# Optimization experiments

Measured on AMD Instinct MI355X. Metric: run time of the kernel, lower is better.

The kernel has to match this reference:

```python
import jax, jax.numpy as jnp
import numpy as np

N_LETTERS = 256
EMBED_DIM = 1024
HIDDEN_DIM = 2048
SEQ_LEN = 4096


def setup_inputs() -> dict:
    key = jax.random.key(0)
    ks = jax.random.split(key, 8)
    s_e = 1.0 / np.sqrt(EMBED_DIM)
    s_h = 1.0 / np.sqrt(HIDDEN_DIM)
    return {
        "input_ids": jax.random.randint(ks[0], (SEQ_LEN,), 0, N_LETTERS, dtype=jnp.int64)
        if jax.config.jax_enable_x64 else jax.random.randint(ks[0], (SEQ_LEN,), 0, N_LETTERS, dtype=jnp.int32),
        "h0": jnp.zeros((1, 1, HIDDEN_DIM), jnp.float32),
        "c0": jnp.zeros((1, 1, HIDDEN_DIM), jnp.float32),
        "W_emb": jax.random.normal(ks[1], (N_LETTERS, EMBED_DIM), jnp.float32),
        "W_ih": jax.random.normal(ks[2], (4 * HIDDEN_DIM, EMBED_DIM), jnp.float32) * s_e,
        "W_hh": jax.random.normal(ks[3], (4 * HIDDEN_DIM, HIDDEN_DIM), jnp.float32) * s_h,
        "b_ih": jnp.zeros((4 * HIDDEN_DIM,), jnp.float32),
        "b_hh": jnp.zeros((4 * HIDDEN_DIM,), jnp.float32),
        "W_out": jax.random.normal(ks[4], (N_LETTERS, HIDDEN_DIM), jnp.float32) * s_h,
        "b_out": jnp.zeros((N_LETTERS,), jnp.float32),
    }


def reference(input_ids, h0, c0, W_emb, W_ih, W_hh, b_ih, b_hh, W_out, b_out):
    H = W_hh.shape[1]
    emb = W_emb[input_ids]                       # [L, E]
    # Precompute the input-side gate projections for all timesteps (batched GEMM).
    x_gates = emb @ W_ih.T + (b_ih + b_hh)       # [L, 4H]

    def step(carry, xg):
        h, c = carry                             # [H], [H]
        gates = xg + W_hh @ h                    # [4H], PyTorch order i,f,g,o
        i = jax.nn.sigmoid(gates[0 * H:1 * H])
        f = jax.nn.sigmoid(gates[1 * H:2 * H])
        g = jnp.tanh(gates[2 * H:3 * H])
        o = jax.nn.sigmoid(gates[3 * H:4 * H])
        c_new = f * c + i * g
        h_new = o * jnp.tanh(c_new)
        return (h_new, c_new), h_new

    (hL, cL), hs = jax.lax.scan(step, (h0[0, 0], c0[0, 0]), x_gates)  # hs: [L, H]
    logits = hs @ W_out.T + b_out                # [L, n_letters]
    # Dropout(p=0.1) is identity in eval mode.
    out = jax.nn.log_softmax(jax.nn.relu(logits), axis=-1)
    return out, hL[None, None, :], cL[None, None, :]
```

## Files before the change

kernel.cpp:

```cpp
#include <hip/hip_runtime.h>
#include <hip/hip_bf16.h>

#define SEQ 4096
#define EMB 1024
#define HID 2048
#define G4  8192
#define NL  256

typedef __attribute__((ext_vector_type(8))) short bf16x8;
typedef __attribute__((ext_vector_type(4))) float f32x4;

static __device__ __forceinline__ unsigned short f2bf(float f) {
    unsigned int x = __builtin_bit_cast(unsigned int, f);
    return (unsigned short)((x + 0x7FFFu + ((x >> 16) & 1u)) >> 16);
}
static __device__ __forceinline__ float bf2f(unsigned short u) {
    return __builtin_bit_cast(float, ((unsigned int)u) << 16);
}

__global__ __launch_bounds__(256) void k_f2b(const float* __restrict__ in,
                                             unsigned short* __restrict__ out, int n) {
    int i = (blockIdx.x * 256 + threadIdx.x) * 4;
    if (i < n) {
        float4 v = *(const float4*)&in[i];
        ushort4 u;
        u.x = f2bf(v.x); u.y = f2bf(v.y); u.z = f2bf(v.z); u.w = f2bf(v.w);
        *(ushort4*)&out[i] = u;
    }
}

__global__ __launch_bounds__(256) void k_emb(const int* __restrict__ ids,
                                             const float* __restrict__ W_emb,
                                             unsigned short* __restrict__ out) {
    int t = blockIdx.x;
    int e0 = threadIdx.x * 4;
    const float4 v = *(const float4*)&W_emb[(size_t)ids[t] * EMB + e0];
    ushort4 u;
    u.x = f2bf(v.x); u.y = f2bf(v.y); u.z = f2bf(v.z); u.w = f2bf(v.w);
    *(ushort4*)&out[(size_t)t * EMB + e0] = u;
}

#define BM 128
#define BN 128
#define BK 32
__global__ __launch_bounds__(256) void k_gemm_bt(
    const unsigned short* __restrict__ A, const unsigned short* __restrict__ B,
    const float* __restrict__ bias1, const float* __restrict__ bias2,
    float* __restrict__ Cf, unsigned short* __restrict__ Cb,
    int M, int N, int K)
{
    __shared__ unsigned short As[BM * BK];
    __shared__ unsigned short Bs[BN * BK];
    const int bm = blockIdx.x * BM;
    const int bn = blockIdx.y * BN;
    const int tid = threadIdx.x;
    const int wave = tid >> 6, lane = tid & 63;
    const int wm = (wave & 1) * 64, wn = (wave >> 1) * 64;
    const int row16 = lane & 15, quad = lane >> 4;

    f32x4 acc[4][4];
#pragma unroll
    for (int i = 0; i < 4; ++i)
#pragma unroll
        for (int j = 0; j < 4; ++j) acc[i][j] = (f32x4){0.f, 0.f, 0.f, 0.f};

    for (int k0 = 0; k0 < K; k0 += BK) {
        __syncthreads();
#pragma unroll
        for (int s = 0; s < 2; ++s) {
            int c = tid + s * 256;
            int r = c >> 2, col = (c & 3) * 8;
            *(uint4*)&As[r * BK + col] = *(const uint4*)&A[(size_t)(bm + r) * K + k0 + col];
            *(uint4*)&Bs[r * BK + col] = *(const uint4*)&B[(size_t)(bn + r) * K + k0 + col];
        }
        __syncthreads();
        bf16x8 af[4], bfr[4];
#pragma unroll
        for (int i = 0; i < 4; ++i) {
            af[i]  = *(const bf16x8*)&As[(wm + i * 16 + row16) * BK + quad * 8];
            bfr[i] = *(const bf16x8*)&Bs[(wn + i * 16 + row16) * BK + quad * 8];
        }
#pragma unroll
        for (int i = 0; i < 4; ++i)
#pragma unroll
            for (int j = 0; j < 4; ++j)
                acc[i][j] = __builtin_amdgcn_mfma_f32_16x16x32_bf16(af[i], bfr[j], acc[i][j], 0, 0, 0);
    }

#pragma unroll
    for (int j = 0; j < 4; ++j) {
        int col = bn + wn + j * 16 + row16;
        float bsum = (bias1 ? bias1[col] : 0.f) + (bias2 ? bias2[col] : 0.f);
#pragma unroll
        for (int i = 0; i < 4; ++i) {
#pragma unroll
            for (int r = 0; r < 4; ++r) {
                int row = bm + wm + i * 16 + quad * 4 + r;
                float v = acc[i][j][r] + bsum;
                if (Cf) Cf[(size_t)row * N + col] = v;
                else    Cb[(size_t)row * N + col] = f2bf(v);
            }
        }
    }
}

#define LSTM_LDS 90112
__global__ __launch_bounds__(1024, 1) void k_lstm(
    const unsigned short* __restrict__ Whhb,
    const unsigned short* __restrict__ xg,
    const float* __restrict__ h0, const float* __restrict__ c0,
    unsigned short* __restrict__ hsb,
    float* __restrict__ outHC,
    unsigned long long* __restrict__ hcomm)
{
    extern __shared__ char smem[];
    unsigned short* hl = (unsigned short*)smem;
    unsigned int*  hl32 = (unsigned int*)smem;
    float* LDSp = (float*)(smem + 4096);
    float* gsum = (float*)(smem + 4096 + 1024);

    const int b = blockIdx.x, tid = threadIdx.x;
    const int wave = tid >> 6, lane = tid & 63;
    const int sub = lane & 15, quad = lane >> 4;
    const int rg = wave & 1, kset = wave >> 1;

    const int q = rg * 2 + (sub >> 3);
    const int j = sub & 7;
    const unsigned short* wsrc =
        Whhb + ((size_t)(q * HID + b * 8 + j)) * HID + kset * 8 * 32 + quad * 8;
    bf16x8 afr[8];
#pragma unroll
    for (int i = 0; i < 8; ++i)
        afr[i] = *(const bf16x8*)(wsrc + i * 32);

    float creg = 0.f;
    if (tid < 8) creg = c0[b * 8 + tid];

    for (int t = 0; t < SEQ; ++t) {
        float xq0 = 0.f, xq1 = 0.f, xq2 = 0.f, xq3 = 0.f;
        if (tid < 8) {
            const unsigned short* xr = xg + (size_t)t * G4 + b * 8 + tid;
            xq0 = bf2f(xr[0]);
            xq1 = bf2f(xr[2048]);
            xq2 = bf2f(xr[4096]);
            xq3 = bf2f(xr[6144]);
        }

        if (t == 0) {
            if (tid < 512) {
                float4 v = *(const float4*)&h0[tid * 4];
                ushort4 u;
                u.x = f2bf(v.x); u.y = f2bf(v.y); u.z = f2bf(v.z); u.w = f2bf(v.w);
                *(ushort4*)&hl[tid * 4] = u;
            }
        } else {
            const unsigned long long* src = hcomm + (size_t)((t - 1) & 1) * 1024;
            const unsigned tag = (unsigned)t;
            unsigned long long x;
            for (;;) {
                x = __hip_atomic_load(&src[tid], __ATOMIC_RELAXED, __HIP_MEMORY_SCOPE_AGENT);
                if ((unsigned)(x >> 32) == tag) break;
                __builtin_amdgcn_s_sleep(1);
            }
            hl32[tid] = (unsigned int)x;
        }
        __syncthreads();

        f32x4 acc0 = (f32x4){0.f, 0.f, 0.f, 0.f};
        f32x4 acc1 = (f32x4){0.f, 0.f, 0.f, 0.f};
#pragma unroll
        for (int i = 0; i < 8; i += 2) {
            bf16x8 h0f = *(const bf16x8*)&hl[(kset * 8 + i) * 32 + quad * 8];
            bf16x8 h1f = *(const bf16x8*)&hl[(kset * 8 + i + 1) * 32 + quad * 8];
            acc0 = __builtin_amdgcn_mfma_f32_16x16x32_bf16(afr[i],     h0f, acc0, 0, 0, 0);
            acc1 = __builtin_amdgcn_mfma_f32_16x16x32_bf16(afr[i + 1], h1f, acc1, 0, 0, 0);
        }
        f32x4 acc = acc0 + acc1;
        if (sub == 0) {
#pragma unroll
            for (int r = 0; r < 4; ++r)
                LDSp[(rg * 16 + quad * 4 + r) * 8 + kset] = acc[r];
        }
        __syncthreads();

        if (tid < 256) {
            float v = LDSp[tid];
            v += __shfl_xor(v, 1); v += __shfl_xor(v, 2); v += __shfl_xor(v, 4);
            if ((tid & 7) == 0) gsum[tid >> 3] = v;
        }
        __syncthreads();

        if (tid < 8) {
            float gi = gsum[tid]      + xq0;
            float gf = gsum[8 + tid]  + xq1;
            float gg = gsum[16 + tid] + xq2;
            float go = gsum[24 + tid] + xq3;
            float i_ = 1.f / (1.f + __expf(-gi));
            float f_ = 1.f / (1.f + __expf(-gf));
            float g_ = tanhf(gg);
            float o_ = 1.f / (1.f + __expf(-go));
            float cn = f_ * creg + i_ * g_;
            float hn = o_ * tanhf(cn);
            creg = cn;
            unsigned hv = (unsigned)f2bf(hn);
            unsigned ov = (unsigned)__shfl_xor((int)hv, 1);
            if ((tid & 1) == 0) {
                unsigned data = hv | (ov << 16);
                __hip_atomic_store(&hcomm[(size_t)(t & 1) * 1024 + b * 4 + (tid >> 1)],
                                   (((unsigned long long)(unsigned)(t + 1)) << 32) | data,
                                   __ATOMIC_RELAXED, __HIP_MEMORY_SCOPE_AGENT);
            }
            hsb[(size_t)t * HID + b * 8 + tid] = f2bf(hn);
            if (t == SEQ - 1) {
                outHC[b * 8 + tid] = hn;
                outHC[HID + b * 8 + tid] = cn;
            }
        }
    }
}

__global__ __launch_bounds__(256) void k_softmax(const float* __restrict__ logits,
                                                 float* __restrict__ out) {
    int row = blockIdx.x * 4 + (threadIdx.x >> 6);
    int lane = threadIdx.x & 63;
    const float* Lr = logits + (size_t)row * NL;
    float4 v = *(const float4*)&Lr[lane * 4];
    v.x = fmaxf(v.x, 0.f); v.y = fmaxf(v.y, 0.f);
    v.z = fmaxf(v.z, 0.f); v.w = fmaxf(v.w, 0.f);
    float m = fmaxf(fmaxf(v.x, v.y), fmaxf(v.z, v.w));
#pragma unroll
    for (int off = 32; off > 0; off >>= 1) m = fmaxf(m, __shfl_xor(m, off));
    float e = __expf(v.x - m) + __expf(v.y - m) + __expf(v.z - m) + __expf(v.w - m);
#pragma unroll
    for (int off = 32; off > 0; off >>= 1) e += __shfl_xor(e, off);
    float ls = __logf(e) + m;
    float4 o;
    o.x = v.x - ls; o.y = v.y - ls; o.z = v.z - ls; o.w = v.w - ls;
    *(float4*)&out[(size_t)row * NL + lane * 4] = o;
}

extern "C" void kernel_launch(void* const* d_in, const int* in_sizes, int n_in,
                              void* d_out, int out_size, void* d_ws, size_t ws_size,
                              hipStream_t stream) {
    const int*   ids   = (const int*)d_in[0];
    const float* h0    = (const float*)d_in[1];
    const float* c0    = (const float*)d_in[2];
    const float* W_emb = (const float*)d_in[3];
    const float* W_ih  = (const float*)d_in[4];
    const float* W_hh  = (const float*)d_in[5];
    const float* b_ih  = (const float*)d_in[6];
    const float* b_hh  = (const float*)d_in[7];
    const float* W_out = (const float*)d_in[8];
    const float* b_out = (const float*)d_in[9];
    float* out = (float*)d_out;

    char* ws = (char*)d_ws;
    unsigned short* xg    = (unsigned short*)(ws);
    unsigned short* hsb   = (unsigned short*)(ws + 67108864);
    unsigned short* Wihb  = (unsigned short*)(ws + 83886080);
    unsigned short* embb  = (unsigned short*)(ws + 100663296);
    unsigned short* Woutb = (unsigned short*)(ws + 109051904);
    float*          logit = (float*)(ws + 110100480);
    unsigned short* Whhb  = (unsigned short*)(ws + 114294784);
    unsigned long long* hcomm = (unsigned long long*)(ws + 147849216);

    k_f2b<<<(G4 * EMB / 4 + 255) / 256, 256, 0, stream>>>(W_ih, Wihb, G4 * EMB);
    k_f2b<<<(NL * HID / 4 + 255) / 256, 256, 0, stream>>>(W_out, Woutb, NL * HID);
    k_f2b<<<(G4 * HID / 4 + 255) / 256, 256, 0, stream>>>(W_hh, Whhb, G4 * HID);
    k_emb<<<SEQ, 256, 0, stream>>>(ids, W_emb, embb);

    dim3 g1(SEQ / BM, G4 / BN);
    k_gemm_bt<<<g1, 256, 0, stream>>>(embb, Wihb, b_ih, b_hh, nullptr, xg, SEQ, G4, EMB);

    hipFuncSetAttribute((const void*)k_lstm, hipFuncAttributeMaxDynamicSharedMemorySize, LSTM_LDS);
    k_lstm<<<256, 1024, LSTM_LDS, stream>>>(Whhb, xg, h0, c0, hsb, out + (size_t)SEQ * NL, hcomm);

    dim3 g2(SEQ / BM, NL / BN);
    k_gemm_bt<<<g2, 256, 0, stream>>>(hsb, Woutb, b_out, nullptr, logit, nullptr, SEQ, NL, HID);

    k_softmax<<<SEQ / 4, 256, 0, stream>>>(logit, out);
}
```

Measured before the change: 11.40 ms.

## Load recurrent h directly into MFMA fragments and cut LSTM step barriers

Each wave now covers a 128-wide K slice for both row groups and polls the tagged hcomm words straight into registers as MFMA B fragments. This removes the LDS staging of h and the barrier that followed it. The cross-wave reduction is merged into a single wave reading padded LDS rows, which drops one __syncthreads per timestep. Gate activations switch to exp-based fast sigmoid and tanh. In exchange, every wave spins on 16 global atomic loads with no sleep, and tanh loses a little accuracy.

```diff
diff --git a/kernel.cpp b/kernel.cpp
--- a/kernel.cpp
+++ b/kernel.cpp
@@ -16,6 +16,15 @@
 }
 static __device__ __forceinline__ float bf2f(unsigned short u) {
     return __builtin_bit_cast(float, ((unsigned int)u) << 16);
+}
+static __device__ __forceinline__ unsigned long long aload(const unsigned long long* p) {
+    return __hip_atomic_load(p, __ATOMIC_RELAXED, __HIP_MEMORY_SCOPE_AGENT);
+}
+static __device__ __forceinline__ float fsigm(float x) {
+    return 1.f / (1.f + __expf(-x));
+}
+static __device__ __forceinline__ float ftanh(float x) {
+    return 1.f - 2.f / (__expf(2.f * x) + 1.f);
 }
 
 __global__ __launch_bounds__(256) void k_f2b(const float* __restrict__ in,
@@ -114,106 +123,131 @@
     unsigned long long* __restrict__ hcomm)
 {
     extern __shared__ char smem[];
-    unsigned short* hl = (unsigned short*)smem;
-    unsigned int*  hl32 = (unsigned int*)smem;
-    float* LDSp = (float*)(smem + 4096);
-    float* gsum = (float*)(smem + 4096 + 1024);
+    float* LDSp = (float*)smem;
 
     const int b = blockIdx.x, tid = threadIdx.x;
     const int wave = tid >> 6, lane = tid & 63;
     const int sub = lane & 15, quad = lane >> 4;
-    const int rg = wave & 1, kset = wave >> 1;
-
-    const int q = rg * 2 + (sub >> 3);
-    const int j = sub & 7;
-    const unsigned short* wsrc =
-        Whhb + ((size_t)(q * HID + b * 8 + j)) * HID + kset * 8 * 32 + quad * 8;
-    bf16x8 afr[8];
-#pragma unroll
-    for (int i = 0; i < 8; ++i)
-        afr[i] = *(const bf16x8*)(wsrc + i * 32);
+
+    const int qa = (sub >> 3), qb = 2 + (sub >> 3), j = sub & 7;
+    const unsigned short* wa = Whhb + ((size_t)(qa * HID + b * 8 + j)) * HID + wave * 128 + quad * 8;
+    const unsigned short* wb = Whhb + ((size_t)(qb * HID + b * 8 + j)) * HID + wave * 128 + quad * 8;
+    bf16x8 afrA[4], afrB[4];
+#pragma unroll
+    for (int c = 0; c < 4; ++c) {
+        afrA[c] = *(const bf16x8*)(wa + c * 32);
+        afrB[c] = *(const bf16x8*)(wb + c * 32);
+    }
 
     float creg = 0.f;
     if (tid < 8) creg = c0[b * 8 + tid];
 
     for (int t = 0; t < SEQ; ++t) {
         float xq0 = 0.f, xq1 = 0.f, xq2 = 0.f, xq3 = 0.f;
-        if (tid < 8) {
-            const unsigned short* xr = xg + (size_t)t * G4 + b * 8 + tid;
+        if (wave == 0 && lane < 8) {
+            const unsigned short* xr = xg + (size_t)t * G4 + b * 8 + lane;
             xq0 = bf2f(xr[0]);
             xq1 = bf2f(xr[2048]);
             xq2 = bf2f(xr[4096]);
             xq3 = bf2f(xr[6144]);
         }
 
-        if (t == 0) {
-            if (tid < 512) {
-                float4 v = *(const float4*)&h0[tid * 4];
-                ushort4 u;
-                u.x = f2bf(v.x); u.y = f2bf(v.y); u.z = f2bf(v.z); u.w = f2bf(v.w);
-                *(ushort4*)&hl[tid * 4] = u;
-            }
-        } else {
-            const unsigned long long* src = hcomm + (size_t)((t - 1) & 1) * 1024;
-            const unsigned tag = (unsigned)t;
-            unsigned long long x;
-            for (;;) {
-                x = __hip_atomic_load(&src[tid], __ATOMIC_RELAXED, __HIP_MEMORY_SCOPE_AGENT);
-                if ((unsigned)(x >> 32) == tag) break;
-                __builtin_amdgcn_s_sleep(1);
-            }
-            hl32[tid] = (unsigned int)x;
-        }
-        __syncthreads();
-
         f32x4 acc0 = (f32x4){0.f, 0.f, 0.f, 0.f};
         f32x4 acc1 = (f32x4){0.f, 0.f, 0.f, 0.f};
-#pragma unroll
-        for (int i = 0; i < 8; i += 2) {
-            bf16x8 h0f = *(const bf16x8*)&hl[(kset * 8 + i) * 32 + quad * 8];
-            bf16x8 h1f = *(const bf16x8*)&hl[(kset * 8 + i + 1) * 32 + quad * 8];
-            acc0 = __builtin_amdgcn_mfma_f32_16x16x32_bf16(afr[i],     h0f, acc0, 0, 0, 0);
-            acc1 = __builtin_amdgcn_mfma_f32_16x16x32_bf16(afr[i + 1], h1f, acc1, 0, 0, 0);
-        }
-        f32x4 acc = acc0 + acc1;
+
+        if (t == 0) {
+#pragma unroll
+            for (int c = 0; c < 4; ++c) {
+                const float* hp = h0 + wave * 128 + c * 32 + quad * 8;
+                float4 va = *(const float4*)hp;
+                float4 vb = *(const float4*)(hp + 4);
+                uint4 d;
+                d.x = (unsigned)f2bf(va.x) | ((unsigned)f2bf(va.y) << 16);
+                d.y = (unsigned)f2bf(va.z) | ((unsigned)f2bf(va.w) << 16);
+                d.z = (unsigned)f2bf(vb.x) | ((unsigned)f2bf(vb.y) << 16);
+                d.w = (unsigned)f2bf(vb.z) | ((unsigned)f2bf(vb.w) << 16);
+                bf16x8 hf = __builtin_bit_cast(bf16x8, d);
+                acc0 = __builtin_amdgcn_mfma_f32_16x16x32_bf16(afrA[c], hf, acc0, 0, 0, 0);
+                acc1 = __builtin_amdgcn_mfma_f32_16x16x32_bf16(afrB[c], hf, acc1, 0, 0, 0);
+            }
+        } else {
+            const unsigned long long* base =
+                hcomm + (size_t)((t - 1) & 1) * 1024 + wave * 64 + quad * 4;
+            const unsigned tag = (unsigned)t;
+            unsigned long long w[16];
+            for (;;) {
+#pragma unroll
+                for (int c = 0; c < 4; ++c)
+#pragma unroll
+                    for (int i = 0; i < 4; ++i)
+                        w[c * 4 + i] = aload(base + c * 16 + i);
+                bool ok = true;
+#pragma unroll
+                for (int k = 0; k < 16; ++k) ok &= ((unsigned)(w[k] >> 32) == tag);
+                if (ok) break;
+            }
+#pragma unroll
+            for (int c = 0; c < 4; ++c) {
+                uint4 d;
+                d.x = (unsigned)w[c * 4 + 0];
+                d.y = (unsigned)w[c * 4 + 1];
+                d.z = (unsigned)w[c * 4 + 2];
+                d.w = (unsigned)w[c * 4 + 3];
+                bf16x8 hf = __builtin_bit_cast(bf16x8, d);
+                acc0 = __builtin_amdgcn_mfma_f32_16x16x32_bf16(afrA[c], hf, acc0, 0, 0, 0);
+                acc1 = __builtin_amdgcn_mfma_f32_16x16x32_bf16(afrB[c], hf, acc1, 0, 0, 0);
+            }
+        }
+
+        __syncthreads();
         if (sub == 0) {
 #pragma unroll
-            for (int r = 0; r < 4; ++r)
-                LDSp[(rg * 16 + quad * 4 + r) * 8 + kset] = acc[r];
+            for (int r = 0; r < 4; ++r) {
+                LDSp[(quad * 4 + r) * 20 + wave]        = acc0[r];
+                LDSp[(16 + quad * 4 + r) * 20 + wave]   = acc1[r];
+            }
         }
         __syncthreads();
 
-        if (tid < 256) {
-            float v = LDSp[tid];
-            v += __shfl_xor(v, 1); v += __shfl_xor(v, 2); v += __shfl_xor(v, 4);
-            if ((tid & 7) == 0) gsum[tid >> 3] = v;
-        }
-        __syncthreads();
-
-        if (tid < 8) {
-            float gi = gsum[tid]      + xq0;
-            float gf = gsum[8 + tid]  + xq1;
-            float gg = gsum[16 + tid] + xq2;
-            float go = gsum[24 + tid] + xq3;
-            float i_ = 1.f / (1.f + __expf(-gi));
-            float f_ = 1.f / (1.f + __expf(-gf));
-            float g_ = tanhf(gg);
-            float o_ = 1.f / (1.f + __expf(-go));
-            float cn = f_ * creg + i_ * g_;
-            float hn = o_ * tanhf(cn);
-            creg = cn;
-            unsigned hv = (unsigned)f2bf(hn);
-            unsigned ov = (unsigned)__shfl_xor((int)hv, 1);
-            if ((tid & 1) == 0) {
-                unsigned data = hv | (ov << 16);
-                __hip_atomic_store(&hcomm[(size_t)(t & 1) * 1024 + b * 4 + (tid >> 1)],
-                                   (((unsigned long long)(unsigned)(t + 1)) << 32) | data,
-                                   __ATOMIC_RELAXED, __HIP_MEMORY_SCOPE_AGENT);
-            }
-            hsb[(size_t)t * HID + b * 8 + tid] = f2bf(hn);
-            if (t == SEQ - 1) {
-                outHC[b * 8 + tid] = hn;
-                outHC[HID + b * 8 + tid] = cn;
+        if (wave == 0) {
+            float g = 0.f;
+            if (lane < 32) {
+                const float* rp = LDSp + lane * 20;
+                f32x4 s = *(const f32x4*)rp;
+                s += *(const f32x4*)(rp + 4);
+                s += *(const f32x4*)(rp + 8);
+                s += *(const f32x4*)(rp + 12);
+                g = s[0] + s[1] + s[2] + s[3];
+            }
+            float gF = __shfl(g, 8 + lane);
+            float gG = __shfl(g, 16 + lane);
+            float gO = __shfl(g, 24 + lane);
+            if (lane < 8) {
+                float gi = g  + xq0;
+                float gf = gF + xq1;
+                float gg = gG + xq2;
+                float go = gO + xq3;
+                float i_ = fsigm(gi);
+                float f_ = fsigm(gf);
+                float g_ = ftanh(gg);
+                float o_ = fsigm(go);
+                float cn = f_ * creg + i_ * g_;
+                float hn = o_ * ftanh(cn);
+                creg = cn;
+                unsigned hv = (unsigned)f2bf(hn);
+                unsigned pv = (unsigned)__shfl((int)hv, lane ^ 1);
+                if (!(lane & 1)) {
+                    unsigned long long wrd =
+                        (((unsigned long long)(unsigned)(t + 1)) << 32)
+                        | (unsigned long long)((pv << 16) | hv);
+                    __hip_atomic_store(&hcomm[(size_t)(t & 1) * 1024 + b * 4 + (lane >> 1)],
+                                       wrd, __ATOMIC_RELAXED, __HIP_MEMORY_SCOPE_AGENT);
+                }
+                hsb[(size_t)t * HID + b * 8 + lane] = (unsigned short)hv;
+                if (t == SEQ - 1) {
+                    outHC[b * 8 + lane] = hn;
+                    outHC[HID + b * 8 + lane] = cn;
+                }
             }
         }
     }
```

Result: slower. 15.26 ms (+33.8%).
